# Kernel tuning notes

Measured on AMD Instinct MI355X. Metric: run time of the kernel, lower is better.

## Reference

```python
import jax, jax.numpy as jnp
import numpy as np

N, D = 4096, 256  # num_nodes, hidden_dim (num_layers = 1)

def setup_inputs() -> dict:
    key = jax.random.key(0)
    ks = jax.random.split(key, 7)
    s = 0.05  # small init scale so the LSTM gates stay in a sane range
    return {
        "h":    jax.random.normal(ks[0], (N, D), dtype=jnp.float32),
        "W_ih": jax.random.normal(ks[1], (4 * D, 2 * D), dtype=jnp.float32) * s,
        "W_hh": jax.random.normal(ks[2], (4 * D, D), dtype=jnp.float32) * s,
        "b_ih": jax.random.normal(ks[3], (4 * D,), dtype=jnp.float32) * s,
        "b_hh": jax.random.normal(ks[4], (4 * D,), dtype=jnp.float32) * s,
        "W_a":  jax.random.normal(ks[5], (D, D), dtype=jnp.float32) * s,
        "b_a":  jax.random.normal(ks[6], (D,), dtype=jnp.float32) * s,
    }

def reference(h, W_ih, W_hh, b_ih, b_hh, W_a, b_a):
    num_nodes, d = h.shape

    def step(carry, _):
        hs, cs, q_star = carry  # hs, cs: (1, D); q_star: (1, 2D)
        # single-layer torch LSTM cell, gate order i, f, g, o
        gates = q_star @ W_ih.T + b_ih + hs @ W_hh.T + b_hh  # (1, 4D)
        i, f, g, o = jnp.split(gates, 4, axis=-1)
        c_new = jax.nn.sigmoid(f) * cs + jax.nn.sigmoid(i) * jnp.tanh(g)
        q = jax.nn.sigmoid(o) * jnp.tanh(c_new)              # (1, D)
        # attention read over all nodes
        e = h @ (q @ W_a.T + b_a)[0]                          # (N,)
        a = jax.nn.softmax(e, axis=0)                         # (N,)
        r = (a @ h)[None, :]                                  # (1, D)
        q_star_new = jnp.concatenate([q, r], axis=-1)         # (1, 2D)
        return (q, c_new, q_star_new), None

    init = (jnp.zeros((1, d), h.dtype), jnp.zeros((1, d), h.dtype),
            jnp.zeros((1, 2 * d), h.dtype))
    (hs, cs, q_star), _ = jax.lax.scan(step, init, None, length=num_nodes)
    return q_star
```

## Files before the change

### kernel.cpp

```cpp
#include <hip/hip_runtime.h>
#include <stdint.h>

#define NN 4096
#define DD 256
#define NWG 64
#define TT 256
#define ROWS 64
#define GR 16
#define NSTEPS 4096
#define GUARD (1u << 20)

typedef float f32x4 __attribute__((ext_vector_type(4)));

#define OFF_HDR      0u
#define OFF_QS       4096u
#define OFF_SCAL     12288u
#define OFF_PR       12352u
#define OFF_EB       77888u
#define OFF_BPACK    94272u
#define OFF_WPACK    98368u
#define OFF_HPB      2195520u
#define OFF_HP2      4292672u

#define S_HPL    0u
#define S_HP     32768u
#define S_WL     65536u
#define S_QRL    98304u
#define S_PRL    100352u
#define S_EL     104448u
#define S_PL     105472u
#define S_GL     105728u
#define S_CLS    105792u
#define S_RED4   105808u
#define S_SL     105824u
#define S_EBL    105840u
#define S_Q4     106096u
#define SMEM_BYTES 106496

__device__ __forceinline__ float bf2f(unsigned short u) {
  return __uint_as_float(((unsigned)u) << 16);
}
__device__ __forceinline__ unsigned short f2bf(float f) {
  unsigned x = __float_as_uint(f);
  unsigned r = x + 0x7fffu + ((x >> 16) & 1u);
  return (unsigned short)(r >> 16);
}

__device__ __forceinline__ f32x4 ld_v4(const void* p) {
  f32x4 v;
  asm volatile("global_load_dwordx4 %0, %1, off sc0 sc1\n\ts_waitcnt vmcnt(0)"
               : "=v"(v) : "v"(p) : "memory");
  return v;
}
__device__ __forceinline__ f32x4 ld_v4_async(const void* p) {
  f32x4 v;
  asm volatile("global_load_dwordx4 %0, %1, off sc0 sc1" : "=v"(v) : "v"(p) : "memory");
  return v;
}
__device__ __forceinline__ void st_v4(void* p, f32x4 v) {
  asm volatile("global_store_dwordx4 %0, %1, off sc0 sc1" :: "v"(p), "v"(v) : "memory");
}
__device__ __forceinline__ void st_f32(void* p, float v) {
  asm volatile("global_store_dword %0, %1, off sc0 sc1" :: "v"(p), "v"(v) : "memory");
}
__device__ __forceinline__ void vmdrain() {
  asm volatile("s_waitcnt vmcnt(0)" ::: "memory");
}

__global__ void k0_init(char* ws) {
  int t = threadIdx.x;
  unsigned* u = (unsigned*)ws;
  float* f = (float*)ws;
  for (int i = t; i < 64; i += TT) {
    u[(OFF_HDR >> 2) + i * 16] = 0u;
    f[(OFF_HDR >> 2) + i * 16 + 1] = 1.0f / NWG;
  }
  for (int i = t; i < 64; i += TT) {
    u[(OFF_QS >> 2) + i * 32] = 0u;
    u[(OFF_QS >> 2) + i * 32 + 16] = 0u;
  }
  if (t == 0) { u[OFF_SCAL / 4] = 0u; u[OFF_SCAL / 4 + 1] = 0u; }
  for (int i = t; i < 64 * 256; i += TT) f[(OFF_PR >> 2) + i] = 0.f;
}

__global__ __launch_bounds__(256) void k1_hp(const float* __restrict__ h,
                                             const float* __restrict__ W_a,
                                             const float* __restrict__ b_a,
                                             char* ws) {
  __shared__ float hL1[16][256];
  __shared__ float scr[16][256];
  __shared__ float redN[4][16];
  __shared__ float redE[4][16];
  const int t = threadIdx.x, b = blockIdx.x;
  const int i0 = b * 16;
  for (int i = t; i < 16 * 256; i += 256) hL1[i >> 8][i & 255] = h[i0 * 256 + i];
  __syncthreads();
  float acc[16];
#pragma unroll
  for (int ii = 0; ii < 16; ++ii) acc[ii] = 0.f;
  for (int j = 0; j < 256; ++j) {
    float wa = W_a[j * 256 + t];
#pragma unroll
    for (int ii = 0; ii < 16; ++ii) acc[ii] += hL1[ii][j] * wa;
  }
#pragma unroll
  for (int ii = 0; ii < 16; ++ii) scr[ii][t] = acc[ii];
  const int lane = t & 63, wv = t >> 6;
  const float ba = b_a[t];
  for (int ii = 0; ii < 16; ++ii) {
    float a2 = acc[ii] * acc[ii];
    float eb = hL1[ii][t] * ba;
    for (int m = 32; m; m >>= 1) { a2 += __shfl_xor(a2, m); eb += __shfl_xor(eb, m); }
    if (lane == 0) { redN[wv][ii] = a2; redE[wv][ii] = eb; }
  }
  __syncthreads();
  unsigned* scal = (unsigned*)(ws + OFF_SCAL);
  float* ebg = (float*)(ws + OFF_EB);
  if (t < 16) {
    float n2 = redN[0][t] + redN[1][t] + redN[2][t] + redN[3][t];
    float ebv = redE[0][t] + redE[1][t] + redE[2][t] + redE[3][t];
    ebg[i0 + t] = ebv;
    atomicMax(scal + 0, __float_as_uint(sqrtf(n2)));
    atomicMax(scal + 1, __float_as_uint(fabsf(ebv)));
  }
  uint2* hpB = (uint2*)(ws + OFF_HPB);
  const int wq = b >> 2, sub = b & 3;
  for (int idx = t; idx < 16 * 64; idx += 256) {
    int ii = idx >> 6, k4 = idx & 63;
    unsigned short u0 = f2bf(scr[ii][4 * k4 + 0]);
    unsigned short u1 = f2bf(scr[ii][4 * k4 + 1]);
    unsigned short u2 = f2bf(scr[ii][4 * k4 + 2]);
    unsigned short u3 = f2bf(scr[ii][4 * k4 + 3]);
    uint2 pv;
    pv.x = (unsigned)u0 | ((unsigned)u1 << 16);
    pv.y = (unsigned)u2 | ((unsigned)u3 << 16);
    int rl = sub * 16 + ii;
    hpB[wq * 4096 + k4 * 64 + rl] = pv;
  }
}

__global__ void k2_pack(const float* __restrict__ h, const float* __restrict__ W_ih,
                        const float* __restrict__ W_hh, const float* __restrict__ b_ih,
                        const float* __restrict__ b_hh, char* ws) {
  unsigned* hp2 = (unsigned*)(ws + OFF_HP2);
  float* wpack = (float*)(ws + OFF_WPACK);
  float* bpack = (float*)(ws + OFF_BPACK);
  int idx0 = blockIdx.x * blockDim.x + threadIdx.x;
  int stride = gridDim.x * blockDim.x;
  for (int i = idx0; i < NN * DD / 2; i += stride) {
    int col = i & 255;
    int r2 = (i >> 8) & 31;
    int w = i >> 13;
    int row0 = (w * 64 + 2 * r2) * 256 + col;
    hp2[i] = (unsigned)f2bf(h[row0]) | ((unsigned)f2bf(h[row0 + 256]) << 16);
  }
  for (int i = idx0; i < 1024 * 512; i += stride) {
    int row = i >> 9, c = i & 511;
    int g = row >> 8, d = row & 255;
    int wq = d >> 2, dl = d & 3;
    float v = W_ih[row * 512 + c];
    if (c < 256) v += W_hh[row * 256 + c];
    wpack[(wq * GR + g * 4 + dl) * 512 + c] = v;
  }
  for (int i = idx0; i < 1024; i += stride) {
    int g = i >> 8, d = i & 255, wq = d >> 2, dl = d & 3;
    bpack[wq * GR + g * 4 + dl] = b_ih[i] + b_hh[i];
  }
}

__global__ __launch_bounds__(TT, 1) void s2s_main(char* __restrict__ ws,
                                                  float* __restrict__ out) {
  extern __shared__ char smem[];
  uint2* HpL = (uint2*)(smem + S_HPL);
  unsigned* hP = (unsigned*)(smem + S_HP);
  float* wL = (float*)(smem + S_WL);
  float* qrL = (float*)(smem + S_QRL);
  float* prL = (float*)(smem + S_PRL);
  float* eL = (float*)(smem + S_EL);
  float* pL = (float*)(smem + S_PL);
  float* gL = (float*)(smem + S_GL);
  float* cLs = (float*)(smem + S_CLS);
  float* red4 = (float*)(smem + S_RED4);
  float* sL = (float*)(smem + S_SL);
  float* ebL = (float*)(smem + S_EBL);
  float* qL4 = (float*)(smem + S_Q4);

  const int w = blockIdx.x, tid = threadIdx.x;
  char* hdrBase = ws + OFF_HDR;
  char* qsBase = ws + OFF_QS;
  const unsigned* scal = (const unsigned*)(ws + OFF_SCAL);
  float* pr = (float*)(ws + OFF_PR);
  const float* ebg = (const float*)(ws + OFF_EB);
  const float* bpack = (const float*)(ws + OFF_BPACK);
  const float* wpack = (const float*)(ws + OFF_WPACK);
  const uint2* hpB = (const uint2*)(ws + OFF_HPB) + (size_t)w * 4096;
  const unsigned* hp2 = (const unsigned*)(ws + OFF_HP2) + (size_t)w * 8192;

  for (int i = tid; i < 4096; i += TT) HpL[i] = hpB[i];
  for (int i = tid; i < 8192; i += TT) hP[i] = hp2[i];
  for (int i = tid; i < 8192; i += TT) wL[i] = wpack[(size_t)w * 8192 + i];
  if (tid < 64) ebL[tid] = ebg[w * 64 + tid];
  if (tid < 4) cLs[tid] = 0.f;
  qrL[tid] = 0.f;
  qrL[256 + tid] = 0.f;
  const float maxHpN = __uint_as_float(scal[0]);
  const float ebB = __uint_as_float(scal[1]);
  __syncthreads();

  const int gr_lr = tid >> 4, gr_li = tid & 15;
  const float* wrow = wL + gr_lr * 512;
  const float brow = bpack[w * GR + gr_lr];
  const int wv4 = tid >> 6, l = tid & 63;
  float psW = 0.f;

  for (int t = 0; t < NSTEPS; ++t) {
    float acc = 0.f;
#pragma unroll
    for (int j = 0; j < 4; ++j) {
      int c0 = gr_li * 4 + j * 64;
      const float4 wv = *(const float4*)(wrow + c0);
      const float4 qv = *(const float4*)(qrL + c0);
      acc += wv.x * qv.x + wv.y * qv.y + wv.z * qv.z + wv.w * qv.w;
    }
    if (tid < 64) {
      const char* hp = hdrBase + tid * 64;
      float psv;
      unsigned guard = 0;
      for (;;) {
        f32x4 hv = ld_v4(hp);
        if (__float_as_uint(hv.x) >= (unsigned)t || ++guard > GUARD) { psv = hv.y; break; }
      }
      float s = psv;
#pragma unroll
      for (int m = 32; m; m >>= 1) s += __shfl_xor(s, m);
      if (tid == 0) sL[0] = fmaxf(s, 1e-35f);
    }
    __syncthreads();
    {
      f32x4 tv[16];
#pragma unroll
      for (int i = 0; i < 16; ++i) {
        int v = (wv4 * 16 + i + w) & 63;
        tv[i] = ld_v4_async(pr + v * 256 + (l << 2));
      }
      vmdrain();
      __builtin_amdgcn_sched_barrier(0);
      float rx = 0.f, ry = 0.f, rz = 0.f, rw = 0.f;
#pragma unroll
      for (int i = 0; i < 16; ++i) { rx += tv[i].x; ry += tv[i].y; rz += tv[i].z; rw += tv[i].w; }
      float* d = prL + wv4 * 256 + (l << 2);
      d[0] = rx; d[1] = ry; d[2] = rz; d[3] = rw;
    }
    __syncthreads();
    {
      float rsum = prL[tid] + prL[256 + tid] + prL[512 + tid] + prL[768 + tid];
      qrL[256 + tid] = rsum / sL[0];
    }
    __syncthreads();
#pragma unroll
    for (int j = 4; j < 8; ++j) {
      int c0 = gr_li * 4 + j * 64;
      const float4 wv = *(const float4*)(wrow + c0);
      const float4 qv = *(const float4*)(qrL + c0);
      acc += wv.x * qv.x + wv.y * qv.y + wv.z * qv.z + wv.w * qv.w;
    }
    acc += __shfl_xor(acc, 8);
    acc += __shfl_xor(acc, 4);
    acc += __shfl_xor(acc, 2);
    acc += __shfl_xor(acc, 1);
    if (gr_li == 0) gL[gr_lr] = acc + brow;
    __syncthreads();
    if (tid < 4) {
      float gi = gL[tid], gf = gL[4 + tid], gg = gL[8 + tid], go = gL[12 + tid];
      float co = cLs[tid];
      float si = 1.f / (1.f + __expf(-gi));
      float sf = 1.f / (1.f + __expf(-gf));
      float so = 1.f / (1.f + __expf(-go));
      float cn = sf * co + si * tanhf(gg);
      cLs[tid] = cn;
      qL4[tid] = so * tanhf(cn);
    }
    __syncthreads();
    if (tid == 0) {
      float4 qv4 = *(const float4*)qL4;
      f32x4 lineA, lineB;
      lineA.x = __uint_as_float((unsigned)(t + 1));
      lineA.y = qv4.x; lineA.z = qv4.y; lineA.w = qv4.z;
      lineB.x = __uint_as_float((unsigned)(t + 1));
      lineB.y = qv4.w; lineB.z = 0.f; lineB.w = 0.f;
      st_v4(qsBase + w * 128, lineA);
      st_v4(qsBase + w * 128 + 64, lineB);
    }

    if (tid < 64) {
      const char* qp = qsBase + tid * 128;
      f32x4 a, b;
      unsigned guard = 0;
      for (;;) {
        a = ld_v4_async(qp);
        b = ld_v4_async(qp + 64);
        vmdrain();
        __builtin_amdgcn_sched_barrier(0);
        unsigned need = (unsigned)(t + 1);
        if ((__float_as_uint(a.x) >= need && __float_as_uint(b.x) >= need) ||
            ++guard > GUARD) break;
      }
      float* qd = qrL + tid * 4;
      qd[0] = a.y; qd[1] = a.z; qd[2] = a.w; qd[3] = b.y;
    }
    __syncthreads();
    float qv = qrL[tid];
    float nr = qv * qv;
#pragma unroll
    for (int m = 32; m; m >>= 1) nr += __shfl_xor(nr, m);
    if (l == 0) red4[wv4] = nr;
    __syncthreads();
    const float qnorm = sqrtf(red4[0] + red4[1] + red4[2] + red4[3]);
    const float Mhat = 0.5f * maxHpN * qnorm + ebB;
    float eacc = 0.f;
#pragma unroll
    for (int j = 0; j < 16; ++j) {
      const int k4 = wv4 * 16 + j;
      const uint2 hp = HpL[(k4 << 6) + l];
      const float* qp = qrL + (k4 << 2);
      eacc += bf2f((unsigned short)(hp.x)) * qp[0] +
              bf2f((unsigned short)(hp.x >> 16)) * qp[1] +
              bf2f((unsigned short)(hp.y)) * qp[2] +
              bf2f((unsigned short)(hp.y >> 16)) * qp[3];
    }
    eL[(wv4 << 6) + l] = eacc;
    __syncthreads();
    if (tid < 64) {
      float e = eL[tid] + eL[64 + tid] + eL[128 + tid] + eL[192 + tid] + ebL[tid];
      float p = __expf(fminf(e - Mhat, 60.f));
      pL[tid] = p;
      float sv = p;
#pragma unroll
      for (int m = 32; m; m >>= 1) sv += __shfl_xor(sv, m);
      if (tid == 0) psW = sv;
    }
    __syncthreads();
    float r2 = 0.f;
#pragma unroll
    for (int r2i = 0; r2i < 32; ++r2i) {
      const unsigned hv = hP[(r2i << 8) + tid];
      r2 += pL[2 * r2i] * bf2f((unsigned short)hv) +
            pL[2 * r2i + 1] * bf2f((unsigned short)(hv >> 16));
    }
    st_f32(pr + (w << 8) + tid, r2);
    vmdrain();
    __syncthreads();
    if (tid == 0) {
      f32x4 hv4;
      hv4.x = __uint_as_float((unsigned)(t + 1));
      hv4.y = psW; hv4.z = 0.f; hv4.w = 0.f;
      st_v4(hdrBase + w * 64, hv4);
    }
  }

  if (w == 0) {
    if (tid < 64) {
      const char* hp = hdrBase + tid * 64;
      float psv;
      unsigned guard = 0;
      for (;;) {
        f32x4 hv = ld_v4(hp);
        if (__float_as_uint(hv.x) >= (unsigned)NSTEPS || ++guard > GUARD) { psv = hv.y; break; }
      }
      float s = psv;
#pragma unroll
      for (int m = 32; m; m >>= 1) s += __shfl_xor(s, m);
      if (tid == 0) sL[0] = fmaxf(s, 1e-35f);
    }
    __syncthreads();
    {
      f32x4 tv[16];
#pragma unroll
      for (int i = 0; i < 16; ++i) {
        int v = (wv4 * 16 + i) & 63;
        tv[i] = ld_v4_async(pr + v * 256 + (l << 2));
      }
      vmdrain();
      __builtin_amdgcn_sched_barrier(0);
      float rx = 0.f, ry = 0.f, rz = 0.f, rw = 0.f;
#pragma unroll
      for (int i = 0; i < 16; ++i) { rx += tv[i].x; ry += tv[i].y; rz += tv[i].z; rw += tv[i].w; }
      float* d = prL + wv4 * 256 + (l << 2);
      d[0] = rx; d[1] = ry; d[2] = rz; d[3] = rw;
    }
    __syncthreads();
    float rsum = prL[tid] + prL[256 + tid] + prL[512 + tid] + prL[768 + tid];
    out[tid] = qrL[tid];
    out[256 + tid] = rsum / sL[0];
  }
}

extern "C" void kernel_launch(void* const* d_in, const int* in_sizes, int n_in,
                              void* d_out, int out_size, void* d_ws, size_t ws_size,
                              hipStream_t stream) {
  const float* h = (const float*)d_in[0];
  const float* W_ih = (const float*)d_in[1];
  const float* W_hh = (const float*)d_in[2];
  const float* b_ih = (const float*)d_in[3];
  const float* b_hh = (const float*)d_in[4];
  const float* W_a = (const float*)d_in[5];
  const float* b_a = (const float*)d_in[6];
  char* ws = (char*)d_ws;
  float* out = (float*)d_out;

  (void)hipFuncSetAttribute(reinterpret_cast<const void*>(s2s_main),
                            hipFuncAttributeMaxDynamicSharedMemorySize, SMEM_BYTES);

  k0_init<<<1, TT, 0, stream>>>(ws);
  k1_hp<<<256, 256, 0, stream>>>(h, W_a, b_a, ws);
  k2_pack<<<1024, 256, 0, stream>>>(h, W_ih, W_hh, b_ih, b_hh, ws);
  s2s_main<<<NWG, TT, SMEM_BYTES, stream>>>(ws, out);
}
```

Measured before the change: 26.31 ms.

## Fuse partial-sum data with step flags to remove separate header polling

Each workgroup's partial attention read vector and softmax denominator are now packed into flagged 16-byte lines (step counter plus three values), so consumers poll the data itself instead of first polling a header and then loading partials. The cross-workgroup reduction becomes a per-wave shuffle reduction over 22 slots, and the q exchange lines are compacted to 32 bytes per group with fewer barriers. The weight tile in LDS is also padded to reduce bank conflicts. The cost is more global loads per step and a wider polling loop over many flag slots.

```diff
diff --git a/kernel.cpp b/kernel.cpp
--- a/kernel.cpp
+++ b/kernel.cpp
@@ -9,33 +9,33 @@
 #define GR 16
 #define NSTEPS 4096
 #define GUARD (1u << 20)
+#define NJ 88
+#define SLOTS 22
 
 typedef float f32x4 __attribute__((ext_vector_type(4)));
 
-#define OFF_HDR      0u
-#define OFF_QS       4096u
-#define OFF_SCAL     12288u
-#define OFF_PR       12352u
-#define OFF_EB       77888u
-#define OFF_BPACK    94272u
-#define OFF_WPACK    98368u
-#define OFF_HPB      2195520u
-#define OFF_HP2      4292672u
+#define OFF_QS       0u
+#define OFF_SCAL     2048u
+#define OFF_PR       4096u
+#define OFF_EB       94208u
+#define OFF_BPACK    110592u
+#define OFF_WPACK    114688u
+#define OFF_HPB      2211840u
+#define OFF_HP2      4308992u
 
 #define S_HPL    0u
 #define S_HP     32768u
 #define S_WL     65536u
-#define S_QRL    98304u
-#define S_PRL    100352u
-#define S_EL     104448u
-#define S_PL     105472u
-#define S_GL     105728u
-#define S_CLS    105792u
-#define S_RED4   105808u
-#define S_SL     105824u
-#define S_EBL    105840u
-#define S_Q4     106096u
-#define SMEM_BYTES 106496
+#define S_QRL    98816u
+#define S_RACC   100864u
+#define S_EL     101952u
+#define S_PL     102976u
+#define S_GL     103232u
+#define S_CLS    103296u
+#define S_RED4   103312u
+#define S_EBL    103328u
+#define S_QL4    103584u
+#define SMEM_BYTES 103680
 
 __device__ __forceinline__ float bf2f(unsigned short u) {
   return __uint_as_float(((unsigned)u) << 16);
@@ -60,27 +60,27 @@
 __device__ __forceinline__ void st_v4(void* p, f32x4 v) {
   asm volatile("global_store_dwordx4 %0, %1, off sc0 sc1" :: "v"(p), "v"(v) : "memory");
 }
-__device__ __forceinline__ void st_f32(void* p, float v) {
-  asm volatile("global_store_dword %0, %1, off sc0 sc1" :: "v"(p), "v"(v) : "memory");
-}
 __device__ __forceinline__ void vmdrain() {
   asm volatile("s_waitcnt vmcnt(0)" ::: "memory");
 }
 
 __global__ void k0_init(char* ws) {
   int t = threadIdx.x;
-  unsigned* u = (unsigned*)ws;
-  float* f = (float*)ws;
-  for (int i = t; i < 64; i += TT) {
-    u[(OFF_HDR >> 2) + i * 16] = 0u;
-    f[(OFF_HDR >> 2) + i * 16 + 1] = 1.0f / NWG;
-  }
-  for (int i = t; i < 64; i += TT) {
-    u[(OFF_QS >> 2) + i * 32] = 0u;
-    u[(OFF_QS >> 2) + i * 32 + 16] = 0u;
-  }
-  if (t == 0) { u[OFF_SCAL / 4] = 0u; u[OFF_SCAL / 4 + 1] = 0u; }
-  for (int i = t; i < 64 * 256; i += TT) f[(OFF_PR >> 2) + i] = 0.f;
+  unsigned* qs = (unsigned*)(ws + OFF_QS);
+  for (int i = t; i < 64 * 8; i += TT) qs[i] = 0u;
+  if (t == 0) {
+    unsigned* sc = (unsigned*)(ws + OFF_SCAL);
+    sc[0] = 0u; sc[1] = 0u;
+  }
+  f32x4* pr = (f32x4*)(ws + OFF_PR);
+  for (int i = t; i < NJ * 64; i += TT) {
+    int j = i >> 6;
+    f32x4 v;
+    v.x = __uint_as_float(0u);
+    v.y = (j == 86) ? (1.0f / NWG) : 0.f;
+    v.z = 0.f; v.w = 0.f;
+    pr[i] = v;
+  }
 }
 
 __global__ __launch_bounds__(256) void k1_hp(const float* __restrict__ h,
@@ -175,21 +175,19 @@
   unsigned* hP = (unsigned*)(smem + S_HP);
   float* wL = (float*)(smem + S_WL);
   float* qrL = (float*)(smem + S_QRL);
-  float* prL = (float*)(smem + S_PRL);
+  float* rAcc = (float*)(smem + S_RACC);
   float* eL = (float*)(smem + S_EL);
   float* pL = (float*)(smem + S_PL);
   float* gL = (float*)(smem + S_GL);
   float* cLs = (float*)(smem + S_CLS);
   float* red4 = (float*)(smem + S_RED4);
-  float* sL = (float*)(smem + S_SL);
   float* ebL = (float*)(smem + S_EBL);
-  float* qL4 = (float*)(smem + S_Q4);
+  float* qL4 = (float*)(smem + S_QL4);
 
   const int w = blockIdx.x, tid = threadIdx.x;
-  char* hdrBase = ws + OFF_HDR;
   char* qsBase = ws + OFF_QS;
+  char* prB = ws + OFF_PR;
   const unsigned* scal = (const unsigned*)(ws + OFF_SCAL);
-  float* pr = (float*)(ws + OFF_PR);
   const float* ebg = (const float*)(ws + OFF_EB);
   const float* bpack = (const float*)(ws + OFF_BPACK);
   const float* wpack = (const float*)(ws + OFF_WPACK);
@@ -198,7 +196,10 @@
 
   for (int i = tid; i < 4096; i += TT) HpL[i] = hpB[i];
   for (int i = tid; i < 8192; i += TT) hP[i] = hp2[i];
-  for (int i = tid; i < 8192; i += TT) wL[i] = wpack[(size_t)w * 8192 + i];
+  for (int i = tid; i < 8192; i += TT) {
+    int r = i >> 9, c = i & 511;
+    wL[r * 520 + c] = wpack[(size_t)w * 8192 + i];
+  }
   if (tid < 64) ebL[tid] = ebg[w * 64 + tid];
   if (tid < 4) cLs[tid] = 0.f;
   qrL[tid] = 0.f;
@@ -208,12 +209,16 @@
   __syncthreads();
 
   const int gr_lr = tid >> 4, gr_li = tid & 15;
-  const float* wrow = wL + gr_lr * 512;
+  const float* wrow = wL + gr_lr * 520;
   const float brow = bpack[w * GR + gr_lr];
   const int wv4 = tid >> 6, l = tid & 63;
   float psW = 0.f;
 
   for (int t = 0; t < NSTEPS; ++t) {
+    f32x4 v[SLOTS];
+#pragma unroll
+    for (int i = 0; i < SLOTS; ++i)
+      v[i] = ld_v4_async(prB + (((i << 8) + tid) << 4));
     float acc = 0.f;
 #pragma unroll
     for (int j = 0; j < 4; ++j) {
@@ -222,39 +227,39 @@
       const float4 qv = *(const float4*)(qrL + c0);
       acc += wv.x * qv.x + wv.y * qv.y + wv.z * qv.z + wv.w * qv.w;
     }
-    if (tid < 64) {
-      const char* hp = hdrBase + tid * 64;
-      float psv;
-      unsigned guard = 0;
+    vmdrain();
+    __builtin_amdgcn_sched_barrier(0);
+    {
+      const unsigned need = (unsigned)t;
+      unsigned ok = 0, guard = 0;
       for (;;) {
-        f32x4 hv = ld_v4(hp);
-        if (__float_as_uint(hv.x) >= (unsigned)t || ++guard > GUARD) { psv = hv.y; break; }
-      }
-      float s = psv;
-#pragma unroll
-      for (int m = 32; m; m >>= 1) s += __shfl_xor(s, m);
-      if (tid == 0) sL[0] = fmaxf(s, 1e-35f);
+#pragma unroll
+        for (int i = 0; i < SLOTS; ++i)
+          if (!(ok & (1u << i)) && __float_as_uint(v[i].x) >= need) ok |= (1u << i);
+        if (ok == 0x3FFFFFu || ++guard > GUARD) break;
+#pragma unroll
+        for (int i = 0; i < SLOTS; ++i)
+          if (!(ok & (1u << i))) v[i] = ld_v4_async(prB + (((i << 8) + tid) << 4));
+        vmdrain();
+        __builtin_amdgcn_sched_barrier(0);
+      }
+    }
+#pragma unroll
+    for (int i = 0; i < SLOTS; ++i) {
+      float a = v[i].y, b = v[i].z, c = v[i].w;
+#pragma unroll
+      for (int m = 1; m < 64; m <<= 1) {
+        a += __shfl_xor(a, m); b += __shfl_xor(b, m); c += __shfl_xor(c, m);
+      }
+      if (l == 0) {
+        int j3 = (4 * i + wv4) * 3;
+        rAcc[j3] = a; rAcc[j3 + 1] = b; rAcc[j3 + 2] = c;
+      }
     }
     __syncthreads();
     {
-      f32x4 tv[16];
-#pragma unroll
-      for (int i = 0; i < 16; ++i) {
-        int v = (wv4 * 16 + i + w) & 63;
-        tv[i] = ld_v4_async(pr + v * 256 + (l << 2));
-      }
-      vmdrain();
-      __builtin_amdgcn_sched_barrier(0);
-      float rx = 0.f, ry = 0.f, rz = 0.f, rw = 0.f;
-#pragma unroll
-      for (int i = 0; i < 16; ++i) { rx += tv[i].x; ry += tv[i].y; rz += tv[i].z; rw += tv[i].w; }
-      float* d = prL + wv4 * 256 + (l << 2);
-      d[0] = rx; d[1] = ry; d[2] = rz; d[3] = rw;
-    }
-    __syncthreads();
-    {
-      float rsum = prL[tid] + prL[256 + tid] + prL[512 + tid] + prL[768 + tid];
-      qrL[256 + tid] = rsum / sL[0];
+      float s = fmaxf(rAcc[258], 1e-35f);
+      qrL[256 + tid] = rAcc[tid] / s;
     }
     __syncthreads();
 #pragma unroll
@@ -280,57 +285,55 @@
       cLs[tid] = cn;
       qL4[tid] = so * tanhf(cn);
     }
-    __syncthreads();
-    if (tid == 0) {
-      float4 qv4 = *(const float4*)qL4;
-      f32x4 lineA, lineB;
-      lineA.x = __uint_as_float((unsigned)(t + 1));
-      lineA.y = qv4.x; lineA.z = qv4.y; lineA.w = qv4.z;
-      lineB.x = __uint_as_float((unsigned)(t + 1));
-      lineB.y = qv4.w; lineB.z = 0.f; lineB.w = 0.f;
-      st_v4(qsBase + w * 128, lineA);
-      st_v4(qsBase + w * 128 + 64, lineB);
-    }
-
-    if (tid < 64) {
-      const char* qp = qsBase + tid * 128;
-      f32x4 a, b;
+    if (tid < 2) {
+      float4 q4 = *(const float4*)qL4;
+      f32x4 line;
+      line.x = __uint_as_float((unsigned)(t + 1));
+      if (tid == 0) { line.y = q4.x; line.z = q4.y; line.w = q4.z; }
+      else          { line.y = q4.w; line.z = 0.f;  line.w = 0.f; }
+      st_v4(qsBase + w * 32 + tid * 16, line);
+    }
+
+    float nr = 0.f;
+    if (l < 32) {
+      const int w2 = (wv4 << 4) + (l >> 1);
+      const char* qp = qsBase + w2 * 32 + (l & 1) * 16;
+      const unsigned need = (unsigned)(t + 1);
+      f32x4 qv;
       unsigned guard = 0;
       for (;;) {
-        a = ld_v4_async(qp);
-        b = ld_v4_async(qp + 64);
-        vmdrain();
-        __builtin_amdgcn_sched_barrier(0);
-        unsigned need = (unsigned)(t + 1);
-        if ((__float_as_uint(a.x) >= need && __float_as_uint(b.x) >= need) ||
-            ++guard > GUARD) break;
-      }
-      float* qd = qrL + tid * 4;
-      qd[0] = a.y; qd[1] = a.z; qd[2] = a.w; qd[3] = b.y;
-    }
-    __syncthreads();
-    float qv = qrL[tid];
-    float nr = qv * qv;
-#pragma unroll
-    for (int m = 32; m; m >>= 1) nr += __shfl_xor(nr, m);
+        qv = ld_v4(qp);
+        if (__float_as_uint(qv.x) >= need || ++guard > GUARD) break;
+      }
+      if ((l & 1) == 0) {
+        qrL[4 * w2] = qv.y; qrL[4 * w2 + 1] = qv.z; qrL[4 * w2 + 2] = qv.w;
+        nr = qv.y * qv.y + qv.z * qv.z + qv.w * qv.w;
+      } else {
+        qrL[4 * w2 + 3] = qv.y;
+        nr = qv.y * qv.y;
+      }
+    }
+#pragma unroll
+    for (int m = 1; m < 64; m <<= 1) nr += __shfl_xor(nr, m);
     if (l == 0) red4[wv4] = nr;
-    __syncthreads();
-    const float qnorm = sqrtf(red4[0] + red4[1] + red4[2] + red4[3]);
-    const float Mhat = 0.5f * maxHpN * qnorm + ebB;
+    f32x4 qk[16];
+#pragma unroll
+    for (int j = 0; j < 16; ++j)
+      qk[j] = *(const f32x4*)(qrL + (wv4 << 6) + (j << 2));
     float eacc = 0.f;
 #pragma unroll
     for (int j = 0; j < 16; ++j) {
-      const int k4 = wv4 * 16 + j;
-      const uint2 hp = HpL[(k4 << 6) + l];
-      const float* qp = qrL + (k4 << 2);
-      eacc += bf2f((unsigned short)(hp.x)) * qp[0] +
-              bf2f((unsigned short)(hp.x >> 16)) * qp[1] +
-              bf2f((unsigned short)(hp.y)) * qp[2] +
-              bf2f((unsigned short)(hp.y >> 16)) * qp[3];
+      const uint2 hp = HpL[(((wv4 << 4) + j) << 6) + l];
+      eacc += bf2f((unsigned short)(hp.x)) * qk[j].x +
+              bf2f((unsigned short)(hp.x >> 16)) * qk[j].y +
+              bf2f((unsigned short)(hp.y)) * qk[j].z +
+              bf2f((unsigned short)(hp.y >> 16)) * qk[j].w;
     }
     eL[(wv4 << 6) + l] = eacc;
     __syncthreads();
     if (tid < 64) {
+      const float qnorm = sqrtf(red4[0] + red4[1] + red4[2] + red4[3]);
+      const float Mhat = 0.5f * maxHpN * qnorm + ebB;
       float e = eL[tid] + eL[64 + tid] + eL[128 + tid] + eL[192 + tid] + ebL[tid];
       float p = __expf(fminf(e - Mhat, 60.f));
       pL[tid] = p;
@@ -347,51 +350,57 @@
       r2 += pL[2 * r2i] * bf2f((unsigned short)hv) +
             pL[2 * r2i + 1] * bf2f((unsigned short)(hv >> 16));
     }
-    st_f32(pr + (w << 8) + tid, r2);
+    rAcc[tid] = r2;
+    if (tid < 8) rAcc[256 + tid] = 0.f;
+    if (tid == 0) rAcc[258] = psW;
+    __syncthreads();
+    if (tid < NJ) {
+      f32x4 line;
+      line.x = __uint_as_float((unsigned)(t + 1));
+      line.y = rAcc[3 * tid];
+      line.z = rAcc[3 * tid + 1];
+      line.w = rAcc[3 * tid + 2];
+      st_v4(prB + ((tid << 6) + w) * 16, line);
+    }
+    __syncthreads();
+  }
+
+  if (w == 0) {
+    f32x4 v[SLOTS];
+    const unsigned need = (unsigned)NSTEPS;
+    unsigned ok = 0, guard = 0;
+#pragma unroll
+    for (int i = 0; i < SLOTS; ++i)
+      v[i] = ld_v4_async(prB + (((i << 8) + tid) << 4));
     vmdrain();
-    __syncthreads();
-    if (tid == 0) {
-      f32x4 hv4;
-      hv4.x = __uint_as_float((unsigned)(t + 1));
-      hv4.y = psW; hv4.z = 0.f; hv4.w = 0.f;
-      st_v4(hdrBase + w * 64, hv4);
-    }
-  }
-
-  if (w == 0) {
-    if (tid < 64) {
-      const char* hp = hdrBase + tid * 64;
-      float psv;
-      unsigned guard = 0;
-      for (;;) {
-        f32x4 hv = ld_v4(hp);
-        if (__float_as_uint(hv.x) >= (unsigned)NSTEPS || ++guard > GUARD) { psv = hv.y; break; }
-      }
-      float s = psv;
-#pragma unroll
-      for (int m = 32; m; m >>= 1) s += __shfl_xor(s, m);
-      if (tid == 0) sL[0] = fmaxf(s, 1e-35f);
-    }
-    __syncthreads();
-    {
-      f32x4 tv[16];
-#pragma unroll
-      for (int i = 0; i < 16; ++i) {
-        int v = (wv4 * 16 + i) & 63;
-        tv[i] = ld_v4_async(pr + v * 256 + (l << 2));
-      }
+    __builtin_amdgcn_sched_barrier(0);
+    for (;;) {
+#pragma unroll
+      for (int i = 0; i < SLOTS; ++i)
+        if (!(ok & (1u << i)) && __float_as_uint(v[i].x) >= need) ok |= (1u << i);
+      if (ok == 0x3FFFFFu || ++guard > GUARD) break;
+#pragma unroll
+      for (int i = 0; i < SLOTS; ++i)
+        if (!(ok & (1u << i))) v[i] = ld_v4_async(prB + (((i << 8) + tid) << 4));
       vmdrain();
       __builtin_amdgcn_sched_barrier(0);
-      float rx = 0.f, ry = 0.f, rz = 0.f, rw = 0.f;
-#pragma unroll
-      for (int i = 0; i < 16; ++i) { rx += tv[i].x; ry += tv[i].y; rz += tv[i].z; rw += tv[i].w; }
-      float* d = prL + wv4 * 256 + (l << 2);
-      d[0] = rx; d[1] = ry; d[2] = rz; d[3] = rw;
-    }
-    __syncthreads();
-    float rsum = prL[tid] + prL[256 + tid] + prL[512 + tid] + prL[768 + tid];
+    }
+#pragma unroll
+    for (int i = 0; i < SLOTS; ++i) {
+      float a = v[i].y, b = v[i].z, c = v[i].w;
+#pragma unroll
+      for (int m = 1; m < 64; m <<= 1) {
+        a += __shfl_xor(a, m); b += __shfl_xor(b, m); c += __shfl_xor(c, m);
+      }
+      if (l == 0) {
+        int j3 = (4 * i + wv4) * 3;
+        rAcc[j3] = a; rAcc[j3 + 1] = b; rAcc[j3 + 2] = c;
+      }
+    }
+    __syncthreads();
+    float s = fmaxf(rAcc[258], 1e-35f);
     out[tid] = qrL[tid];
-    out[256 + tid] = rsum / sL[0];
+    out[256 + tid] = rAcc[tid] / s;
   }
 }
 
```

After: 52.97 ms. +101.3%, slower.

## Distribute per-wave q polling, drop barriers, pad weight rows, vectorize partial stores

Applied to the files above, without the earlier changes.

In the per-step exchange of the LSTM output between workgroups, each wave now polls and loads only the 16 workgroups' q slices it needs for its own part of the attention dot product. This removes two workgroup-wide barriers and moves the norm reduction off the critical barrier path. Weight rows in LDS are padded from 512 to 520 floats to cut bank conflicts. Partial r vectors are staged through LDS so they go out as dwordx4 stores from 64 lanes instead of scalar stores from all threads. Spin loops gain an s_sleep, which eases memory pressure from polling but may add wake-up latency on the critical path.

```diff
diff --git a/kernel.cpp b/kernel.cpp
--- a/kernel.cpp
+++ b/kernel.cpp
@@ -25,17 +25,18 @@
 #define S_HPL    0u
 #define S_HP     32768u
 #define S_WL     65536u
-#define S_QRL    98304u
-#define S_PRL    100352u
-#define S_EL     104448u
-#define S_PL     105472u
-#define S_GL     105728u
-#define S_CLS    105792u
-#define S_RED4   105808u
-#define S_SL     105824u
-#define S_EBL    105840u
-#define S_Q4     106096u
-#define SMEM_BYTES 106496
+#define S_QRL    98816u
+#define S_PRL    100864u
+#define S_RACC   104960u
+#define S_EL     106048u
+#define S_PL     107072u
+#define S_GL     107328u
+#define S_CLS    107392u
+#define S_RED4   107408u
+#define S_SL     107424u
+#define S_EBL    107440u
+#define S_QL4    107696u
+#define SMEM_BYTES 107712
 
 __device__ __forceinline__ float bf2f(unsigned short u) {
   return __uint_as_float(((unsigned)u) << 16);
@@ -60,12 +61,10 @@
 __device__ __forceinline__ void st_v4(void* p, f32x4 v) {
   asm volatile("global_store_dwordx4 %0, %1, off sc0 sc1" :: "v"(p), "v"(v) : "memory");
 }
-__device__ __forceinline__ void st_f32(void* p, float v) {
-  asm volatile("global_store_dword %0, %1, off sc0 sc1" :: "v"(p), "v"(v) : "memory");
-}
 __device__ __forceinline__ void vmdrain() {
   asm volatile("s_waitcnt vmcnt(0)" ::: "memory");
 }
+__device__ __forceinline__ void npause() { __builtin_amdgcn_s_sleep(1); }
 
 __global__ void k0_init(char* ws) {
   int t = threadIdx.x;
@@ -176,6 +175,7 @@
   float* wL = (float*)(smem + S_WL);
   float* qrL = (float*)(smem + S_QRL);
   float* prL = (float*)(smem + S_PRL);
+  float* rAcc = (float*)(smem + S_RACC);
   float* eL = (float*)(smem + S_EL);
   float* pL = (float*)(smem + S_PL);
   float* gL = (float*)(smem + S_GL);
@@ -183,7 +183,7 @@
   float* red4 = (float*)(smem + S_RED4);
   float* sL = (float*)(smem + S_SL);
   float* ebL = (float*)(smem + S_EBL);
-  float* qL4 = (float*)(smem + S_Q4);
+  float* qL4 = (float*)(smem + S_QL4);
 
   const int w = blockIdx.x, tid = threadIdx.x;
   char* hdrBase = ws + OFF_HDR;
@@ -198,7 +198,10 @@
 
   for (int i = tid; i < 4096; i += TT) HpL[i] = hpB[i];
   for (int i = tid; i < 8192; i += TT) hP[i] = hp2[i];
-  for (int i = tid; i < 8192; i += TT) wL[i] = wpack[(size_t)w * 8192 + i];
+  for (int i = tid; i < 8192; i += TT) {
+    int r = i >> 9, c = i & 511;
+    wL[r * 520 + c] = wpack[(size_t)w * 8192 + i];
+  }
   if (tid < 64) ebL[tid] = ebg[w * 64 + tid];
   if (tid < 4) cLs[tid] = 0.f;
   qrL[tid] = 0.f;
@@ -208,7 +211,7 @@
   __syncthreads();
 
   const int gr_lr = tid >> 4, gr_li = tid & 15;
-  const float* wrow = wL + gr_lr * 512;
+  const float* wrow = wL + gr_lr * 520;
   const float brow = bpack[w * GR + gr_lr];
   const int wv4 = tid >> 6, l = tid & 63;
   float psW = 0.f;
@@ -229,6 +232,7 @@
       for (;;) {
         f32x4 hv = ld_v4(hp);
         if (__float_as_uint(hv.x) >= (unsigned)t || ++guard > GUARD) { psv = hv.y; break; }
+        npause();
       }
       float s = psv;
 #pragma unroll
@@ -280,57 +284,56 @@
       cLs[tid] = cn;
       qL4[tid] = so * tanhf(cn);
     }
-    __syncthreads();
-    if (tid == 0) {
-      float4 qv4 = *(const float4*)qL4;
-      f32x4 lineA, lineB;
-      lineA.x = __uint_as_float((unsigned)(t + 1));
-      lineA.y = qv4.x; lineA.z = qv4.y; lineA.w = qv4.z;
-      lineB.x = __uint_as_float((unsigned)(t + 1));
-      lineB.y = qv4.w; lineB.z = 0.f; lineB.w = 0.f;
-      st_v4(qsBase + w * 128, lineA);
-      st_v4(qsBase + w * 128 + 64, lineB);
-    }
-
-    if (tid < 64) {
-      const char* qp = qsBase + tid * 128;
-      f32x4 a, b;
+    if (tid < 2) {
+      float4 q4 = *(const float4*)qL4;
+      f32x4 line;
+      line.x = __uint_as_float((unsigned)(t + 1));
+      if (tid == 0) { line.y = q4.x; line.z = q4.y; line.w = q4.z; }
+      else          { line.y = q4.w; line.z = 0.f;  line.w = 0.f; }
+      st_v4(qsBase + w * 128 + tid * 64, line);
+    }
+
+    float nr = 0.f;
+    if (l < 32) {
+      const int w2 = (wv4 << 4) + (l >> 1);
+      const char* qp = qsBase + w2 * 128 + (l & 1) * 64;
+      const unsigned need = (unsigned)(t + 1);
+      f32x4 qv;
       unsigned guard = 0;
       for (;;) {
-        a = ld_v4_async(qp);
-        b = ld_v4_async(qp + 64);
-        vmdrain();
-        __builtin_amdgcn_sched_barrier(0);
-        unsigned need = (unsigned)(t + 1);
-        if ((__float_as_uint(a.x) >= need && __float_as_uint(b.x) >= need) ||
-            ++guard > GUARD) break;
-      }
-      float* qd = qrL + tid * 4;
-      qd[0] = a.y; qd[1] = a.z; qd[2] = a.w; qd[3] = b.y;
-    }
-    __syncthreads();
-    float qv = qrL[tid];
-    float nr = qv * qv;
-#pragma unroll
-    for (int m = 32; m; m >>= 1) nr += __shfl_xor(nr, m);
+        qv = ld_v4(qp);
+        if (__float_as_uint(qv.x) >= need || ++guard > GUARD) break;
+        npause();
+      }
+      if ((l & 1) == 0) {
+        qrL[4 * w2] = qv.y; qrL[4 * w2 + 1] = qv.z; qrL[4 * w2 + 2] = qv.w;
+        nr = qv.y * qv.y + qv.z * qv.z + qv.w * qv.w;
+      } else {
+        qrL[4 * w2 + 3] = qv.y;
+        nr = qv.y * qv.y;
+      }
+    }
+#pragma unroll
+    for (int m = 1; m < 64; m <<= 1) nr += __shfl_xor(nr, m);
     if (l == 0) red4[wv4] = nr;
-    __syncthreads();
-    const float qnorm = sqrtf(red4[0] + red4[1] + red4[2] + red4[3]);
-    const float Mhat = 0.5f * maxHpN * qnorm + ebB;
+    f32x4 qk[16];
+#pragma unroll
+    for (int j = 0; j < 16; ++j)
+      qk[j] = *(const f32x4*)(qrL + (wv4 << 6) + (j << 2));
     float eacc = 0.f;
 #pragma unroll
     for (int j = 0; j < 16; ++j) {
-      const int k4 = wv4 * 16 + j;
-      const uint2 hp = HpL[(k4 << 6) + l];
-      const float* qp = qrL + (k4 << 2);
-      eacc += bf2f((unsigned short)(hp.x)) * qp[0] +
-              bf2f((unsigned short)(hp.x >> 16)) * qp[1] +
-              bf2f((unsigned short)(hp.y)) * qp[2] +
-              bf2f((unsigned short)(hp.y >> 16)) * qp[3];
+      const uint2 hp = HpL[(((wv4 << 4) + j) << 6) + l];
+      eacc += bf2f((unsigned short)(hp.x)) * qk[j].x +
+              bf2f((unsigned short)(hp.x >> 16)) * qk[j].y +
+              bf2f((unsigned short)(hp.y)) * qk[j].z +
+              bf2f((unsigned short)(hp.y >> 16)) * qk[j].w;
     }
     eL[(wv4 << 6) + l] = eacc;
     __syncthreads();
     if (tid < 64) {
+      const float qnorm = sqrtf(red4[0] + red4[1] + red4[2] + red4[3]);
+      const float Mhat = 0.5f * maxHpN * qnorm + ebB;
       float e = eL[tid] + eL[64 + tid] + eL[128 + tid] + eL[192 + tid] + ebL[tid];
       float p = __expf(fminf(e - Mhat, 60.f));
       pL[tid] = p;
@@ -347,8 +350,15 @@
       r2 += pL[2 * r2i] * bf2f((unsigned short)hv) +
             pL[2 * r2i + 1] * bf2f((unsigned short)(hv >> 16));
     }
-    st_f32(pr + (w << 8) + tid, r2);
-    vmdrain();
+    rAcc[tid] = r2;
+    __syncthreads();
+    if (tid < 64) {
+      f32x4 pv;
+      pv.x = rAcc[4 * tid]; pv.y = rAcc[4 * tid + 1];
+      pv.z = rAcc[4 * tid + 2]; pv.w = rAcc[4 * tid + 3];
+      st_v4(pr + (w << 8) + (tid << 2), pv);
+      vmdrain();
+    }
     __syncthreads();
     if (tid == 0) {
       f32x4 hv4;
@@ -366,6 +376,7 @@
       for (;;) {
         f32x4 hv = ld_v4(hp);
         if (__float_as_uint(hv.x) >= (unsigned)NSTEPS || ++guard > GUARD) { psv = hv.y; break; }
+        npause();
       }
       float s = psv;
 #pragma unroll
```

New measurement: 25.19 ms. 1.04x faster.
